# Performance work log

Measured on AMD Instinct MI355X. Metric: run time of the kernel, lower is better.

Reference implementation:

```python
import jax, jax.numpy as jnp
import numpy as np

S = 4096   # sequence length == max_length
L = 16     # CHAR_LENGTH
F = 256    # char feature size == word-embed size (hidden_size kwarg)
H = 512    # LSTM hidden = 2 * hidden_size kwarg
V = 44     # char vocab from build_char_lang()


def setup_inputs() -> dict:
    key = jax.random.key(0)
    ks = jax.random.split(key, 12)
    def rn(k, shape, s=0.05):
        return jax.random.normal(k, shape, jnp.float32) * s
    return {
        "word_embeddings": rn(ks[0], (S, F), 1.0),
        "char_idxs": jax.random.randint(ks[1], (S, L), 0, V),
        "char_embed": rn(ks[2], (V, F), 1.0),
        "conv_w": rn(ks[3], (F, 2, F)),           # [out_ch, kh=2, kw=F]
        "conv_b": jnp.zeros((F,), jnp.float32),
        "lin_w": rn(ks[4], (F, F)),
        "lin_b": jnp.zeros((F,), jnp.float32),
        "Wih_f": rn(ks[5], (4 * H, H)),
        "Whh_f": rn(ks[6], (4 * H, H)),
        "bih_f": jnp.zeros((4 * H,), jnp.float32),
        "bhh_f": jnp.zeros((4 * H,), jnp.float32),
        "Wih_r": rn(ks[7], (4 * H, H)),
        "Whh_r": rn(ks[8], (4 * H, H)),
        "bih_r": jnp.zeros((4 * H,), jnp.float32),
        "bhh_r": jnp.zeros((4 * H,), jnp.float32),
    }


def _lstm(x, Wih, Whh, bih, bhh):
    """PyTorch-convention single-layer LSTM over leading axis of x [T, H]."""
    Hh = Whh.shape[1]
    b = bih + bhh
    def step(carry, xt):
        h, c = carry
        g = xt @ Wih.T + h @ Whh.T + b          # [4H]
        i, f, gg, o = jnp.split(g, 4)
        c = jax.nn.sigmoid(f) * c + jax.nn.sigmoid(i) * jnp.tanh(gg)
        h = jax.nn.sigmoid(o) * jnp.tanh(c)
        return (h, c), h
    z = jnp.zeros((Hh,), x.dtype)
    (h, c), ys = jax.lax.scan(step, (z, z), x)
    return ys, h, c


def _char_cnn(char_idxs, char_embed, conv_w, conv_b, lin_w, lin_b):
    ce = char_embed[char_idxs]                          # [S, L, F]
    win = jnp.stack([ce[:, :-1, :], ce[:, 1:, :]], 2)    # [S, L-1, 2, F]
    conv = jnp.einsum('slkf,okf->slo', win, conv_w) + conv_b  # [S, L-1, F]
    pooled = jnp.max(jax.nn.relu(conv), axis=1)          # maxpool over L-1 -> [S, F]
    return pooled @ lin_w.T + lin_b                      # [S, F]


def reference(word_embeddings, char_idxs, char_embed, conv_w, conv_b, lin_w, lin_b,
              Wih_f, Whh_f, bih_f, bhh_f, Wih_r, Whh_r, bih_r, bhh_r):
    char_feat = _char_cnn(char_idxs, char_embed, conv_w, conv_b, lin_w, lin_b)
    x = jnp.concatenate([word_embeddings, char_feat], axis=1)   # [S, H]
    fwd_out, hf, cf = _lstm(x, Wih_f, Whh_f, bih_f, bhh_f)
    rev_out, hr, cr = _lstm(x[::-1], Wih_r, Whh_r, bih_r, bhh_r)
    outputs = jnp.concatenate([fwd_out, rev_out[::-1]], axis=1)  # [S, 2H]
    hidden = jnp.concatenate([hf, hr])                           # [2H]
    cell = jnp.concatenate([cf, cr])                             # [2H]
    return outputs, hidden, cell
```

## Files before the change

kernel.cpp:

```cpp
#include <hip/hip_runtime.h>
#include <cstdint>

#define SQ 4096
#define FD 256
#define HD 512
#define GD 2048

#define WS_X       0
#define WS_XPROJ   (WS_X + SQ*HD)
#define WS_WT      (WS_XPROJ + 2*SQ*GD)
#define WS_LINT    (WS_WT + 2*FD*FD)
#define WS_SYNC    (WS_LINT + FD*FD)

typedef __attribute__((ext_vector_type(4))) float f32x4;
typedef unsigned long long u64;

__device__ __forceinline__ float sigf(float x) { return 1.f / (1.f + __expf(-x)); }
__device__ __forceinline__ float tanh_s(float x) { return fmaf(2.f, sigf(2.f * x), -1.f); }

#define REP8(M) M(0)M(1)M(2)M(3)M(4)M(5)M(6)M(7)

__global__ __launch_bounds__(256) void prep_kernel(const float* __restrict__ conv_w,
                                                   const float* __restrict__ lin_w,
                                                   float* __restrict__ Wt,
                                                   float* __restrict__ linT,
                                                   float* __restrict__ sync) {
  int n = blockIdx.x * 256 + threadIdx.x;
  if (n < 4096) sync[n] = 0.f;
  if (n < 2 * FD * FD) {
    int o = n & 255, f = (n >> 8) & 255, k = n >> 16;
    Wt[n] = conv_w[o * 512 + k * 256 + f];
  } else {
    int m = n - 2 * FD * FD;
    int o = m & 255, f = m >> 8;
    linT[m] = lin_w[o * 256 + f];
  }
}

__global__ __launch_bounds__(256) void charcnn_kernel(const float* __restrict__ wemb,
    const int* __restrict__ cidx, const float* __restrict__ cemb,
    const float* __restrict__ Wt, const float* __restrict__ conv_b,
    const float* __restrict__ linT, const float* __restrict__ lin_b,
    float* __restrict__ x) {
  __shared__ float ceT[256][20];
  __shared__ float pooled[256];
  int s = blockIdx.x, o = threadIdx.x;
  #pragma unroll
  for (int l = 0; l < 16; ++l) {
    int idx = cidx[s * 16 + l];
    ceT[o][l] = cemb[idx * 256 + o];
  }
  __syncthreads();
  float acc[15];
  float cb = conv_b[o];
  #pragma unroll
  for (int l = 0; l < 15; ++l) acc[l] = cb;
  for (int f = 0; f < 256; ++f) {
    float w0 = Wt[f * 256 + o];
    float w1 = Wt[65536 + f * 256 + o];
    float4 ca = *(const float4*)&ceT[f][0];
    float4 cv = *(const float4*)&ceT[f][4];
    float4 cc = *(const float4*)&ceT[f][8];
    float4 cd = *(const float4*)&ceT[f][12];
    float c[16] = {ca.x, ca.y, ca.z, ca.w, cv.x, cv.y, cv.z, cv.w,
                   cc.x, cc.y, cc.z, cc.w, cd.x, cd.y, cd.z, cd.w};
    #pragma unroll
    for (int l = 0; l < 15; ++l) acc[l] += c[l] * w0 + c[l + 1] * w1;
  }
  float m = 0.f;
  #pragma unroll
  for (int l = 0; l < 15; ++l) m = fmaxf(m, acc[l]);
  pooled[o] = m;
  __syncthreads();
  float a2 = lin_b[o];
  for (int f = 0; f < 256; f += 4) {
    float4 p = *(const float4*)&pooled[f];
    a2 += p.x * linT[(f + 0) * 256 + o] + p.y * linT[(f + 1) * 256 + o]
        + p.z * linT[(f + 2) * 256 + o] + p.w * linT[(f + 3) * 256 + o];
  }
  x[(size_t)s * 512 + o] = wemb[(size_t)s * 256 + o];
  x[(size_t)s * 512 + 256 + o] = a2;
}

__global__ __launch_bounds__(256) void xproj_kernel(const float* __restrict__ x,
    const float* __restrict__ Wih_f, const float* __restrict__ Wih_r,
    const float* __restrict__ bih_f, const float* __restrict__ bhh_f,
    const float* __restrict__ bih_r, const float* __restrict__ bhh_r,
    float* __restrict__ xproj) {
  __shared__ float As[64][33];
  __shared__ float Bs[64][33];
  int dir = blockIdx.z;
  const float* B  = dir ? Wih_r : Wih_f;
  const float* b1 = dir ? bih_r : bih_f;
  const float* b2 = dir ? bhh_r : bhh_f;
  int m0 = blockIdx.x * 64, n0 = blockIdx.y * 64;
  int tid = threadIdx.x, tx = tid & 15, ty = tid >> 4;
  float acc[4][4];
  #pragma unroll
  for (int j = 0; j < 4; ++j) {
    float bias = b1[n0 + tx * 4 + j] + b2[n0 + tx * 4 + j];
    #pragma unroll
    for (int i = 0; i < 4; ++i) acc[i][j] = bias;
  }
  int lc = tid & 31, lr0 = tid >> 5;
  for (int k0 = 0; k0 < 512; k0 += 32) {
    #pragma unroll
    for (int i = 0; i < 8; ++i) {
      As[lr0 + 8 * i][lc] = x[(size_t)(m0 + lr0 + 8 * i) * 512 + k0 + lc];
      Bs[lr0 + 8 * i][lc] = B[(size_t)(n0 + lr0 + 8 * i) * 512 + k0 + lc];
    }
    __syncthreads();
    #pragma unroll
    for (int kk = 0; kk < 32; ++kk) {
      float a0 = As[ty * 4 + 0][kk], a1 = As[ty * 4 + 1][kk];
      float a2 = As[ty * 4 + 2][kk], a3 = As[ty * 4 + 3][kk];
      float q0 = Bs[tx * 4 + 0][kk], q1 = Bs[tx * 4 + 1][kk];
      float q2 = Bs[tx * 4 + 2][kk], q3 = Bs[tx * 4 + 3][kk];
      acc[0][0] += a0 * q0; acc[0][1] += a0 * q1; acc[0][2] += a0 * q2; acc[0][3] += a0 * q3;
      acc[1][0] += a1 * q0; acc[1][1] += a1 * q1; acc[1][2] += a1 * q2; acc[1][3] += a1 * q3;
      acc[2][0] += a2 * q0; acc[2][1] += a2 * q1; acc[2][2] += a2 * q2; acc[2][3] += a2 * q3;
      acc[3][0] += a3 * q0; acc[3][1] += a3 * q1; acc[3][2] += a3 * q2; acc[3][3] += a3 * q3;
    }
    __syncthreads();
  }
  size_t base = (size_t)dir * SQ * GD;
  #pragma unroll
  for (int i = 0; i < 4; ++i) {
    float4 v = make_float4(acc[i][0], acc[i][1], acc[i][2], acc[i][3]);
    *(float4*)&xproj[base + (size_t)(m0 + ty * 4 + i) * GD + n0 + tx * 4] = v;
  }
}

__global__ __launch_bounds__(1024, 4) void lstm_kernel(const float* __restrict__ xproj,
    const float* __restrict__ Whh_f, const float* __restrict__ Whh_r,
    u64* __restrict__ payu, float* __restrict__ out) {
  __shared__ float h4[16 * 36];
  __shared__ float g_lds[64];
  int dir = blockIdx.x >> 5;
  int wid = blockIdx.x & 31;
  int hbase = wid * 16;
  int tid = threadIdx.x;

  int r = tid >> 4, kq = tid & 15;
  int Rrow = ((r >> 4) << 9) + hbase + (r & 15);
  const float* Whh = dir ? Whh_r : Whh_f;
  const float* xp = xproj + (size_t)dir * SQ * GD;
  const f32x4* wsrc4 = (const f32x4*)(Whh + (size_t)Rrow * 512 + kq * 32);
#define LDW(i) f32x4 w##i = wsrc4[i];
  REP8(LDW)
#undef LDW
#define PIN(i) asm volatile("" : "+v"(w##i));
  REP8(PIN)
#undef PIN

  float cst = 0.f, hlast = 0.f;

  for (int t = 0; t < SQ; ++t) {
    int p = dir ? (SQ - 1 - t) : t;
    float xval = 0.f;
    if (kq == 0) xval = xp[(size_t)p * GD + Rrow];
    if (tid < 256) {
      float v0, v1;
      if (t == 0) { v0 = 0.f; v1 = 0.f; }
      else {
        const u64* src = payu + (((size_t)(dir * 2 + ((t - 1) & 1)) * 256) + tid) * 2;
        unsigned tg = (unsigned)t;
        for (;;) {
          u64 lo = __hip_atomic_load(src,     __ATOMIC_RELAXED, __HIP_MEMORY_SCOPE_AGENT);
          u64 hi = __hip_atomic_load(src + 1, __ATOMIC_RELAXED, __HIP_MEMORY_SCOPE_AGENT);
          if ((unsigned)lo == tg && (unsigned)(hi >> 32) == tg) {
            v0 = __uint_as_float((unsigned)(lo >> 32));
            v1 = __uint_as_float((unsigned)hi);
            break;
          }
          __builtin_amdgcn_s_sleep(1);
        }
      }
      int ih = tid * 2;
      int sl = ih >> 5, off = ih & 31;
      h4[sl * 36 + off] = v0;
      h4[sl * 36 + off + 1] = v1;
    }
    __syncthreads();
    float a0 = 0.f, a1 = 0.f, a2 = 0.f, a3 = 0.f;
    const f32x4* hq4 = (const f32x4*)&h4[kq * 36];
#define GST(i) { f32x4 hh = hq4[i]; \
    a0 = fmaf(w##i[0], hh[0], a0); a1 = fmaf(w##i[1], hh[1], a1); \
    a2 = fmaf(w##i[2], hh[2], a2); a3 = fmaf(w##i[3], hh[3], a3); }
    REP8(GST)
#undef GST
    float acc = (a0 + a1) + (a2 + a3);
    acc += __shfl_xor(acc, 1);
    acc += __shfl_xor(acc, 2);
    acc += __shfl_xor(acc, 4);
    acc += __shfl_xor(acc, 8);
    if (kq == 0) g_lds[r] = acc + xval;
    __syncthreads();
    if (tid < 16) {
      float ig = g_lds[tid], fg = g_lds[16 + tid], gg = g_lds[32 + tid], og = g_lds[48 + tid];
      float c = sigf(fg) * cst + sigf(ig) * tanh_s(gg);
      float hval = sigf(og) * tanh_s(c);
      cst = c; hlast = hval;
      out[(size_t)p * 1024 + dir * 512 + hbase + tid] = hval;
      unsigned tg = (unsigned)(t + 1);
      u64 word = (tid & 1) ? (((u64)tg << 32) | __float_as_uint(hval))
                           : (((u64)__float_as_uint(hval) << 32) | tg);
      u64* dst = payu + (((size_t)(dir * 2 + (t & 1)) * 256) + wid * 8 + (tid >> 1)) * 2 + (tid & 1);
      u64 old = __hip_atomic_exchange(dst, word, __ATOMIC_RELAXED, __HIP_MEMORY_SCOPE_AGENT);
      asm volatile("" :: "v"(old));
    }
  }
  if (tid < 16) {
    size_t OH = (size_t)SQ * 1024;
    out[OH + dir * 512 + hbase + tid] = hlast;
    out[OH + 1024 + dir * 512 + hbase + tid] = cst;
  }
}

extern "C" void kernel_launch(void* const* d_in, const int* in_sizes, int n_in,
                              void* d_out, int out_size, void* d_ws, size_t ws_size,
                              hipStream_t stream) {
  const float* wemb   = (const float*)d_in[0];
  const int*   cidx   = (const int*)d_in[1];
  const float* cemb   = (const float*)d_in[2];
  const float* conv_w = (const float*)d_in[3];
  const float* conv_b = (const float*)d_in[4];
  const float* lin_w  = (const float*)d_in[5];
  const float* lin_b  = (const float*)d_in[6];
  const float* Wih_f  = (const float*)d_in[7];
  const float* Whh_f  = (const float*)d_in[8];
  const float* bih_f  = (const float*)d_in[9];
  const float* bhh_f  = (const float*)d_in[10];
  const float* Wih_r  = (const float*)d_in[11];
  const float* Whh_r  = (const float*)d_in[12];
  const float* bih_r  = (const float*)d_in[13];
  const float* bhh_r  = (const float*)d_in[14];
  float* out = (float*)d_out;
  float* ws = (float*)d_ws;
  float* x     = ws + WS_X;
  float* xproj = ws + WS_XPROJ;
  float* Wt    = ws + WS_WT;
  float* linT  = ws + WS_LINT;
  float* sync  = ws + WS_SYNC;

  prep_kernel<<<768, 256, 0, stream>>>(conv_w, lin_w, Wt, linT, sync);
  charcnn_kernel<<<SQ, 256, 0, stream>>>(wemb, cidx, cemb, Wt, conv_b, linT, lin_b, x);
  xproj_kernel<<<dim3(64, 32, 2), 256, 0, stream>>>(x, Wih_f, Wih_r, bih_f, bhh_f, bih_r, bhh_r, xproj);
  lstm_kernel<<<64, 1024, 0, stream>>>(xproj, Whh_f, Whh_r, (u64*)sync, out);
}
```

Measured before the change: 7.639 ms.

## Remap LSTM gates per wavefront to drop a barrier and simplify flag polling

Each wavefront now owns one hidden unit, holding all four gates across its 64 lanes. Gate activations are gathered with shuffles instead of going through LDS, which removes the second __syncthreads per timestep. The h-exchange payload becomes one 64-bit word per hidden value, each carrying its own step tag, so 512 threads each poll a single word without s_sleep. The LDS h buffer is double-buffered so one barrier per step suffices. The cost is more polling threads and tighter spin loops hitting the same cache lines.

New measurement: 7.476 ms (median of 2 runs). -2.1%, faster.

```diff
diff --git a/kernel.cpp b/kernel.cpp
--- a/kernel.cpp
+++ b/kernel.cpp
@@ -134,15 +134,14 @@
 __global__ __launch_bounds__(1024, 4) void lstm_kernel(const float* __restrict__ xproj,
     const float* __restrict__ Whh_f, const float* __restrict__ Whh_r,
     u64* __restrict__ payu, float* __restrict__ out) {
-  __shared__ float h4[16 * 36];
-  __shared__ float g_lds[64];
+  __shared__ float hl[2][16 * 36];
   int dir = blockIdx.x >> 5;
   int wid = blockIdx.x & 31;
   int hbase = wid * 16;
   int tid = threadIdx.x;
-
-  int r = tid >> 4, kq = tid & 15;
-  int Rrow = ((r >> 4) << 9) + hbase + (r & 15);
+  int w = tid >> 6, lane = tid & 63;
+  int gate = lane >> 4, kq = lane & 15;
+  int Rrow = (gate << 9) + hbase + w;
   const float* Whh = dir ? Whh_r : Whh_f;
   const float* xp = xproj + (size_t)dir * SQ * GD;
   const f32x4* wsrc4 = (const f32x4*)(Whh + (size_t)Rrow * 512 + kq * 32);
@@ -152,38 +151,32 @@
 #define PIN(i) asm volatile("" : "+v"(w##i));
   REP8(PIN)
 #undef PIN
-
+  u64* mypay = payu + (size_t)dir * 1024;
+
+  const bool lz = (lane == 0);
   float cst = 0.f, hlast = 0.f;
 
   for (int t = 0; t < SQ; ++t) {
     int p = dir ? (SQ - 1 - t) : t;
     float xval = 0.f;
     if (kq == 0) xval = xp[(size_t)p * GD + Rrow];
-    if (tid < 256) {
-      float v0, v1;
-      if (t == 0) { v0 = 0.f; v1 = 0.f; }
+    int buf = (t + 1) & 1;
+    if (tid < 512) {
+      float hv;
+      if (t == 0) hv = 0.f;
       else {
-        const u64* src = payu + (((size_t)(dir * 2 + ((t - 1) & 1)) * 256) + tid) * 2;
+        const u64* src = mypay + ((t - 1) & 1) * 512 + tid;
         unsigned tg = (unsigned)t;
-        for (;;) {
-          u64 lo = __hip_atomic_load(src,     __ATOMIC_RELAXED, __HIP_MEMORY_SCOPE_AGENT);
-          u64 hi = __hip_atomic_load(src + 1, __ATOMIC_RELAXED, __HIP_MEMORY_SCOPE_AGENT);
-          if ((unsigned)lo == tg && (unsigned)(hi >> 32) == tg) {
-            v0 = __uint_as_float((unsigned)(lo >> 32));
-            v1 = __uint_as_float((unsigned)hi);
-            break;
-          }
-          __builtin_amdgcn_s_sleep(1);
-        }
+        u64 v;
+        do { v = __hip_atomic_load(src, __ATOMIC_RELAXED, __HIP_MEMORY_SCOPE_AGENT); }
+        while ((unsigned)(v >> 32) != tg);
+        hv = __uint_as_float((unsigned)v);
       }
-      int ih = tid * 2;
-      int sl = ih >> 5, off = ih & 31;
-      h4[sl * 36 + off] = v0;
-      h4[sl * 36 + off + 1] = v1;
+      hl[buf][(tid >> 5) * 36 + (tid & 31)] = hv;
     }
     __syncthreads();
     float a0 = 0.f, a1 = 0.f, a2 = 0.f, a3 = 0.f;
-    const f32x4* hq4 = (const f32x4*)&h4[kq * 36];
+    const f32x4* hq4 = (const f32x4*)&hl[buf][kq * 36];
 #define GST(i) { f32x4 hh = hq4[i]; \
     a0 = fmaf(w##i[0], hh[0], a0); a1 = fmaf(w##i[1], hh[1], a1); \
     a2 = fmaf(w##i[2], hh[2], a2); a3 = fmaf(w##i[3], hh[3], a3); }
@@ -194,26 +187,27 @@
     acc += __shfl_xor(acc, 2);
     acc += __shfl_xor(acc, 4);
     acc += __shfl_xor(acc, 8);
-    if (kq == 0) g_lds[r] = acc + xval;
-    __syncthreads();
-    if (tid < 16) {
-      float ig = g_lds[tid], fg = g_lds[16 + tid], gg = g_lds[32 + tid], og = g_lds[48 + tid];
-      float c = sigf(fg) * cst + sigf(ig) * tanh_s(gg);
-      float hval = sigf(og) * tanh_s(c);
+    float gx = acc + xval;
+    float act = (gate == 2) ? tanh_s(gx) : sigf(gx);
+    float aI = __shfl(act, 0);
+    float aF = __shfl(act, 16);
+    float aG = __shfl(act, 32);
+    float aO = __shfl(act, 48);
+    if (lz) {
+      float c = aF * cst + aI * aG;
+      float hval = aO * tanh_s(c);
       cst = c; hlast = hval;
-      out[(size_t)p * 1024 + dir * 512 + hbase + tid] = hval;
-      unsigned tg = (unsigned)(t + 1);
-      u64 word = (tid & 1) ? (((u64)tg << 32) | __float_as_uint(hval))
-                           : (((u64)__float_as_uint(hval) << 32) | tg);
-      u64* dst = payu + (((size_t)(dir * 2 + (t & 1)) * 256) + wid * 8 + (tid >> 1)) * 2 + (tid & 1);
-      u64 old = __hip_atomic_exchange(dst, word, __ATOMIC_RELAXED, __HIP_MEMORY_SCOPE_AGENT);
+      u64 word = ((u64)(unsigned)(t + 1) << 32) | __float_as_uint(hval);
+      u64 old = __hip_atomic_exchange(mypay + (t & 1) * 512 + hbase + w, word,
+                                      __ATOMIC_RELAXED, __HIP_MEMORY_SCOPE_AGENT);
       asm volatile("" :: "v"(old));
-    }
-  }
-  if (tid < 16) {
+      out[(size_t)p * 1024 + dir * 512 + hbase + w] = hval;
+    }
+  }
+  if (lz) {
     size_t OH = (size_t)SQ * 1024;
-    out[OH + dir * 512 + hbase + tid] = hlast;
-    out[OH + 1024 + dir * 512 + hbase + tid] = cst;
+    out[OH + dir * 512 + hbase + w] = hlast;
+    out[OH + 1024 + dir * 512 + hbase + w] = cst;
   }
 }
 
```
